# Kernel tuning notes

Hardware: AMD Instinct MI355X
Metric: run time of the kernel (lower is better)

## Reference

```python
import jax, jax.numpy as jnp
import numpy as np

CAUSAL = True


def setup_inputs() -> dict:
    key = jax.random.key(0)
    k1, k2, k3 = jax.random.split(key, 3)
    B, H, T, D = 2, 16, 2048, 64
    q = jax.random.normal(k1, (B, H, T, D), dtype=jnp.float32)
    k = jax.random.normal(k2, (B, H, T, D), dtype=jnp.float32)
    v = jax.random.normal(k3, (B, H, T, D), dtype=jnp.float32)
    return {"q": q, "k": k, "v": v}


def reference(q, k, v):
    # q,k,v: [B,H,T,D]
    d = q.shape[-1]
    scale = d ** -0.5
    dots = jnp.einsum('bhid,bhjd->bhij', q, k) * scale  # [B,H,T,T]
    if CAUSAL:
        t = q.shape[2]
        mask = jnp.triu(jnp.ones((t, t), dtype=bool), k=1)  # True above diagonal
        dots = jnp.where(mask, -jnp.inf, dots)
    attn = jax.nn.softmax(dots, axis=-1)
    # torch.einsum('bhjd,bhij->bhid', v, attn) == attn @ v
    return jnp.einsum('bhij,bhjd->bhid', attn, v)
```

## Files before the change

### kernel.cpp

```cpp
#include <hip/hip_runtime.h>
#include <hip/hip_bf16.h>

typedef unsigned short u16;
typedef unsigned int u32;
typedef __bf16 bf16x8 __attribute__((ext_vector_type(8)));
typedef short s16x4 __attribute__((ext_vector_type(4)));
typedef short s16x8 __attribute__((ext_vector_type(8)));
typedef float floatx4 __attribute__((ext_vector_type(4)));

#define T_SEQ 2048
#define HDIM 64
#define NBH 32

static __device__ __forceinline__ u16 f2b_rne(float x) {
    union { float f; u32 u; } c; c.f = x;
    u32 u = c.u;
    return (u16)((u + 0x7fffu + ((u >> 16) & 1u)) >> 16);
}
static __device__ __forceinline__ u16 f2b_trunc(float x) {
    union { float f; u32 u; } c; c.f = x;
    return (u16)(c.u >> 16);
}

#define GLOAD_LDS16(gp, lp)                                                      \
    __builtin_amdgcn_global_load_lds(                                            \
        (const __attribute__((address_space(1))) u32*)(gp),                      \
        (__attribute__((address_space(3))) u32*)(lp), 16, 0, 0)

__global__ __launch_bounds__(256) void prep(const float* __restrict__ k,
                                            const float* __restrict__ v,
                                            u16* __restrict__ kb,
                                            u16* __restrict__ vt) {
    __shared__ u16 tile[64][68];
    const int bh = blockIdx.y, t0 = blockIdx.x * 64;
    const int tid = threadIdx.x;

    const float* ksrc = k + ((size_t)bh * T_SEQ + t0) * HDIM;
    u16* kdst = kb + ((size_t)bh * T_SEQ + t0) * HDIM;
#pragma unroll
    for (int p = 0; p < 4; p++) {
        int idx = p * 256 + tid;
        float4 f = ((const float4*)ksrc)[idx];
        ushort4 o;
        o.x = f2b_rne(f.x); o.y = f2b_rne(f.y); o.z = f2b_rne(f.z); o.w = f2b_rne(f.w);
        ((ushort4*)kdst)[idx] = o;
    }

    const float* vsrc = v + ((size_t)bh * T_SEQ + t0) * HDIM;
#pragma unroll
    for (int p = 0; p < 4; p++) {
        int idx = p * 256 + tid;
        int r = idx >> 4, c4 = (idx & 15) * 4;
        float4 f = *(const float4*)(vsrc + r * HDIM + c4);
        tile[c4 + 0][r] = f2b_rne(f.x);
        tile[c4 + 1][r] = f2b_rne(f.y);
        tile[c4 + 2][r] = f2b_rne(f.z);
        tile[c4 + 3][r] = f2b_rne(f.w);
    }
    __syncthreads();
    u16* dst = vt + (size_t)bh * HDIM * T_SEQ + t0;
#pragma unroll
    for (int p = 0; p < 4; p++) {
        int idx = p * 256 + tid;
        int d = idx >> 4, c4 = (idx & 15) * 4;
        int t = c4 >> 4, qg = (c4 >> 2) & 3;
        int pos = qg * 16 + (t >> 1) * 8 + (t & 1) * 4;
        *(ushort4*)(dst + (size_t)d * T_SEQ + pos) = *(ushort4*)(&tile[d][c4]);
    }
}

__global__ __launch_bounds__(256, 2) void fattn(const float* __restrict__ q,
                                                const u16* __restrict__ kb,
                                                const u16* __restrict__ vtb,
                                                float* __restrict__ out) {
    __shared__ __align__(16) u16 Kl[2][64 * 64];
    __shared__ __align__(16) u16 Vl[2][64 * 64];

    const int bh = blockIdx.x;
    const int sr = blockIdx.y;
    const int st = (sr < 8) ? (2 * sr) : (2 * (15 - sr) + 1);
    const int tid = threadIdx.x;
    const int wave = tid >> 6, lane = tid & 63;
    const int l15 = lane & 15, quad = lane >> 4;

    const float* qp = q + (size_t)bh * T_SEQ * HDIM;
    const u16* kp = kb + (size_t)bh * T_SEQ * HDIM;
    const u16* vp = vtb + (size_t)bh * HDIM * T_SEQ;

    const int iters = 2 * st + 2;
    const int w32 = wave * 32;

    const int srow = wave * 8 + (lane >> 3);
    const int slot = lane & 7;
    const u16* kg0 = kp + srow * HDIM + (slot ^ (srow & 7)) * 8;
    const int vs = (slot - srow) & 7;
    const u16* vg0 = vp + (size_t)srow * T_SEQ + vs * 8;
    const u16* vg1 = vp + (size_t)(srow + 32) * T_SEQ + vs * 8;

    auto stage = [&](int j, int buf) {
        const u16* ks = kg0 + j * 64 * HDIM;
        u16* Kd = &Kl[buf][wave * 512];
        GLOAD_LDS16(ks, Kd);
        GLOAD_LDS16(ks + 32 * HDIM, Kd + 2048);
        u16* Vd = &Vl[buf][wave * 512];
        GLOAD_LDS16(vg0 + j * 64, Vd);
        GLOAD_LDS16(vg1 + j * 64, Vd + 2048);
    };

    stage(0, 0);

    const float SL2E = 0.125f * 1.44269504088896f;
    bf16x8 qf[2][2];
#pragma unroll
    for (int qn = 0; qn < 2; qn++) {
        const float* qrow = qp + (size_t)(st * 128 + w32 + qn * 16 + l15) * HDIM;
#pragma unroll
        for (int kc = 0; kc < 2; kc++) {
            const float4* p4 = (const float4*)(qrow + kc * 32 + quad * 8);
            float4 fa = p4[0], fb = p4[1];
            union { bf16x8 v; u16 s[8]; } cv;
            cv.s[0] = f2b_rne(fa.x * SL2E); cv.s[1] = f2b_rne(fa.y * SL2E);
            cv.s[2] = f2b_rne(fa.z * SL2E); cv.s[3] = f2b_rne(fa.w * SL2E);
            cv.s[4] = f2b_rne(fb.x * SL2E); cv.s[5] = f2b_rne(fb.y * SL2E);
            cv.s[6] = f2b_rne(fb.z * SL2E); cv.s[7] = f2b_rne(fb.w * SL2E);
            qf[qn][kc] = cv.v;
        }
    }

    floatx4 o_acc[2][4];
#pragma unroll
    for (int qn = 0; qn < 2; qn++)
#pragma unroll
        for (int dt = 0; dt < 4; dt++) o_acc[qn][dt] = (floatx4){0.f, 0.f, 0.f, 0.f};
    float lsum[2] = {0.f, 0.f};

    for (int j = 0; j < iters; ++j) {
        const int cur = j & 1;
        __syncthreads();

        if (j + 1 < iters) stage(j + 1, cur ^ 1);

        const int rel = j * 64 - st * 128;
        if (rel <= w32 + 31) {
            floatx4 sacc[2][4];
#pragma unroll
            for (int qn = 0; qn < 2; qn++)
#pragma unroll
                for (int kt = 0; kt < 4; kt++) sacc[qn][kt] = (floatx4){0.f, 0.f, 0.f, 0.f};
            const u16* Kc = Kl[cur];
#pragma unroll
            for (int kc = 0; kc < 2; kc++) {
#pragma unroll
                for (int kt = 0; kt < 4; kt++) {
                    int rk = kt * 16 + l15;
                    bf16x8 kf = *(const bf16x8*)(Kc + rk * 64 + ((kc * 4 + quad) ^ (rk & 7)) * 8);
                    sacc[0][kt] = __builtin_amdgcn_mfma_f32_16x16x32_bf16(kf, qf[0][kc], sacc[0][kt], 0, 0, 0);
                    sacc[1][kt] = __builtin_amdgcn_mfma_f32_16x16x32_bf16(kf, qf[1][kc], sacc[1][kt], 0, 0, 0);
                }
            }

            s16x4 pfrag[2][4];
            if (rel + 63 >= w32) {
#pragma unroll
                for (int qn = 0; qn < 2; qn++) {
                    const int gq = w32 + qn * 16 + l15;
#pragma unroll
                    for (int kt = 0; kt < 4; kt++) {
                        union { s16x4 v; u16 h[4]; } pk;
#pragma unroll
                        for (int rg = 0; rg < 4; rg++) {
                            float e = __builtin_amdgcn_exp2f(sacc[qn][kt][rg]);
                            if (rel + kt * 16 + quad * 4 + rg > gq) e = 0.f;
                            lsum[qn] += e;
                            pk.h[rg] = f2b_trunc(e);
                        }
                        pfrag[qn][kt] = pk.v;
                    }
                }
            } else {
#pragma unroll
                for (int qn = 0; qn < 2; qn++)
#pragma unroll
                    for (int kt = 0; kt < 4; kt++) {
                        union { s16x4 v; u16 h[4]; } pk;
#pragma unroll
                        for (int rg = 0; rg < 4; rg++) {
                            float e = __builtin_amdgcn_exp2f(sacc[qn][kt][rg]);
                            lsum[qn] += e;
                            pk.h[rg] = f2b_trunc(e);
                        }
                        pfrag[qn][kt] = pk.v;
                    }
            }

            const u16* Vc = Vl[cur];
#pragma unroll
            for (int tp = 0; tp < 2; tp++) {
#pragma unroll
                for (int dt = 0; dt < 4; dt++) {
                    int d = dt * 16 + l15;
                    int sl = (quad * 2 + tp + d) & 7;
                    s16x8 vf = *(const s16x8*)(Vc + d * 64 + sl * 8);
                    s16x4 vf0 = __builtin_shufflevector(vf, vf, 0, 1, 2, 3);
                    s16x4 vf1 = __builtin_shufflevector(vf, vf, 4, 5, 6, 7);
                    o_acc[0][dt] = __builtin_amdgcn_mfma_f32_16x16x16bf16_1k(pfrag[0][2 * tp], vf0, o_acc[0][dt], 0, 0, 0);
                    o_acc[0][dt] = __builtin_amdgcn_mfma_f32_16x16x16bf16_1k(pfrag[0][2 * tp + 1], vf1, o_acc[0][dt], 0, 0, 0);
                    o_acc[1][dt] = __builtin_amdgcn_mfma_f32_16x16x16bf16_1k(pfrag[1][2 * tp], vf0, o_acc[1][dt], 0, 0, 0);
                    o_acc[1][dt] = __builtin_amdgcn_mfma_f32_16x16x16bf16_1k(pfrag[1][2 * tp + 1], vf1, o_acc[1][dt], 0, 0, 0);
                }
            }
        }
    }

    float* op = out + (size_t)bh * T_SEQ * HDIM;
#pragma unroll
    for (int qn = 0; qn < 2; qn++) {
        float tot = lsum[qn];
        tot += __shfl_xor(tot, 16, 64);
        tot += __shfl_xor(tot, 32, 64);
#pragma unroll
        for (int rg = 0; rg < 4; rg++) {
            float inv = 1.0f / __shfl(tot, quad * 4 + rg, 64);
            size_t row = (size_t)(st * 128 + w32 + qn * 16 + quad * 4 + rg) * HDIM;
#pragma unroll
            for (int dt = 0; dt < 4; dt++)
                op[row + dt * 16 + l15] = o_acc[qn][dt][rg] * inv;
        }
    }
}

extern "C" void kernel_launch(void* const* d_in, const int* in_sizes, int n_in,
                              void* d_out, int out_size, void* d_ws, size_t ws_size,
                              hipStream_t stream) {
    const float* q = (const float*)d_in[0];
    const float* k = (const float*)d_in[1];
    const float* v = (const float*)d_in[2];
    float* out = (float*)d_out;

    u16* kb = (u16*)d_ws;
    u16* vt = kb + (size_t)NBH * T_SEQ * HDIM;

    prep<<<dim3(T_SEQ / 64, NBH), 256, 0, stream>>>(k, v, kb, vt);
    fattn<<<dim3(NBH, 16), 256, 0, stream>>>(q, kb, vt, out);
}
```

Before: 131.6 us.

## Split KV windows across waves with per-wave pipelines and LDS reduction

Each block now handles a 64-row query tile. Its four waves split the key/value sequence into interleaved 32-key windows instead of splitting the query rows. Each wave runs its own double-buffered global-to-LDS pipeline synchronised with waitcnt, so no block barriers are needed in the main loop, and the partial outputs and row sums are reduced through LDS at the end. The grid doubles to 32 query tiles per head, scheduled largest-first, and the V transpose layout changes to 32-key windows. This aims to remove per-iteration __syncthreads stalls and improve load balance. It costs a larger LDS footprint and an extra cross-wave reduction.

Result: faster. 124.2 us (-5.6%).

```diff
diff --git a/kernel.cpp b/kernel.cpp
--- a/kernel.cpp
+++ b/kernel.cpp
@@ -63,8 +63,8 @@
     for (int p = 0; p < 4; p++) {
         int idx = p * 256 + tid;
         int d = idx >> 4, c4 = (idx & 15) * 4;
-        int t = c4 >> 4, qg = (c4 >> 2) & 3;
-        int pos = qg * 16 + (t >> 1) * 8 + (t & 1) * 4;
+        int win = c4 >> 5, kt = (c4 >> 4) & 1, qg = (c4 >> 2) & 3;
+        int pos = win * 32 + qg * 8 + kt * 4;
         *(ushort4*)(dst + (size_t)d * T_SEQ + pos) = *(ushort4*)(&tile[d][c4]);
     }
 }
@@ -73,12 +73,10 @@
                                                 const u16* __restrict__ kb,
                                                 const u16* __restrict__ vtb,
                                                 float* __restrict__ out) {
-    __shared__ __align__(16) u16 Kl[2][64 * 64];
-    __shared__ __align__(16) u16 Vl[2][64 * 64];
+    __shared__ __align__(16) u16 smem[35328];
 
     const int bh = blockIdx.x;
-    const int sr = blockIdx.y;
-    const int st = (sr < 8) ? (2 * sr) : (2 * (15 - sr) + 1);
+    const int qt = 31 - (int)blockIdx.y;
     const int tid = threadIdx.x;
     const int wave = tid >> 6, lane = tid & 63;
     const int l15 = lane & 15, quad = lane >> 4;
@@ -87,33 +85,36 @@
     const u16* kp = kb + (size_t)bh * T_SEQ * HDIM;
     const u16* vp = vtb + (size_t)bh * HDIM * T_SEQ;
 
-    const int iters = 2 * st + 2;
-    const int w32 = wave * 32;
-
-    const int srow = wave * 8 + (lane >> 3);
-    const int slot = lane & 7;
-    const u16* kg0 = kp + srow * HDIM + (slot ^ (srow & 7)) * 8;
-    const int vs = (slot - srow) & 7;
-    const u16* vg0 = vp + (size_t)srow * T_SEQ + vs * 8;
-    const u16* vg1 = vp + (size_t)(srow + 32) * T_SEQ + vs * 8;
-
-    auto stage = [&](int j, int buf) {
-        const u16* ks = kg0 + j * 64 * HDIM;
-        u16* Kd = &Kl[buf][wave * 512];
-        GLOAD_LDS16(ks, Kd);
-        GLOAD_LDS16(ks + 32 * HDIM, Kd + 2048);
-        u16* Vd = &Vl[buf][wave * 512];
-        GLOAD_LDS16(vg0 + j * 64, Vd);
-        GLOAD_LDS16(vg1 + j * 64, Vd + 2048);
+    const int nwin = 2 * qt + 2;
+    const int nmy = (nwin > wave) ? ((nwin - wave + 3) >> 2) : 0;
+
+    u16* Tb = smem + wave * 8192;
+
+    const int ln3 = lane >> 3, ln7 = lane & 7;
+    const int ln2 = lane >> 2, ln3m = lane & 3;
+
+    auto stage = [&](int win, int b) {
+        const u16* ks = kp + win * 32 * HDIM;
+        u16* Kd = Tb + b * 2048;
+#pragma unroll
+        for (int l = 0; l < 4; l++) {
+            int kr = l * 8 + ln3;
+            GLOAD_LDS16(ks + kr * HDIM + (ln7 ^ (kr & 7)) * 8, Kd + l * 512);
+        }
+        const u16* vs = vp + win * 32;
+        u16* Vd = Tb + 4096 + b * 2048;
+#pragma unroll
+        for (int l = 0; l < 4; l++) {
+            int dr = l * 16 + ln2;
+            GLOAD_LDS16(vs + (size_t)dr * T_SEQ + ((ln3m - dr) & 3) * 8, Vd + l * 512);
+        }
     };
 
-    stage(0, 0);
-
     const float SL2E = 0.125f * 1.44269504088896f;
-    bf16x8 qf[2][2];
-#pragma unroll
-    for (int qn = 0; qn < 2; qn++) {
-        const float* qrow = qp + (size_t)(st * 128 + w32 + qn * 16 + l15) * HDIM;
+    bf16x8 qf[4][2];
+#pragma unroll
+    for (int qn = 0; qn < 4; qn++) {
+        const float* qrow = qp + (size_t)(qt * 64 + qn * 16 + l15) * HDIM;
 #pragma unroll
         for (int kc = 0; kc < 2; kc++) {
             const float4* p4 = (const float4*)(qrow + kc * 32 + quad * 8);
@@ -126,105 +127,140 @@
             qf[qn][kc] = cv.v;
         }
     }
-
-    floatx4 o_acc[2][4];
-#pragma unroll
-    for (int qn = 0; qn < 2; qn++)
+    asm volatile("s_waitcnt vmcnt(0)" ::: "memory");
+
+    if (nmy > 0) stage(wave, 0);
+    if (nmy > 1) stage(wave + 4, 1);
+
+    floatx4 o_acc[4][4];
+#pragma unroll
+    for (int qn = 0; qn < 4; qn++)
 #pragma unroll
         for (int dt = 0; dt < 4; dt++) o_acc[qn][dt] = (floatx4){0.f, 0.f, 0.f, 0.f};
-    float lsum[2] = {0.f, 0.f};
-
-    for (int j = 0; j < iters; ++j) {
-        const int cur = j & 1;
-        __syncthreads();
-
-        if (j + 1 < iters) stage(j + 1, cur ^ 1);
-
-        const int rel = j * 64 - st * 128;
-        if (rel <= w32 + 31) {
-            floatx4 sacc[2][4];
-#pragma unroll
-            for (int qn = 0; qn < 2; qn++)
-#pragma unroll
-                for (int kt = 0; kt < 4; kt++) sacc[qn][kt] = (floatx4){0.f, 0.f, 0.f, 0.f};
-            const u16* Kc = Kl[cur];
-#pragma unroll
-            for (int kc = 0; kc < 2; kc++) {
-#pragma unroll
-                for (int kt = 0; kt < 4; kt++) {
-                    int rk = kt * 16 + l15;
-                    bf16x8 kf = *(const bf16x8*)(Kc + rk * 64 + ((kc * 4 + quad) ^ (rk & 7)) * 8);
-                    sacc[0][kt] = __builtin_amdgcn_mfma_f32_16x16x32_bf16(kf, qf[0][kc], sacc[0][kt], 0, 0, 0);
-                    sacc[1][kt] = __builtin_amdgcn_mfma_f32_16x16x32_bf16(kf, qf[1][kc], sacc[1][kt], 0, 0, 0);
+    float lsum[4] = {0.f, 0.f, 0.f, 0.f};
+
+    for (int i = 0; i < nmy; i++) {
+        const int win = wave + 4 * i;
+        const int b = i & 1;
+        if (i + 1 < nmy) { asm volatile("s_waitcnt vmcnt(8)" ::: "memory"); }
+        else             { asm volatile("s_waitcnt vmcnt(0)" ::: "memory"); }
+
+        const u16* Kc = Tb + b * 2048;
+        bf16x8 kf[2][2];
+#pragma unroll
+        for (int kt = 0; kt < 2; kt++) {
+            int kr = kt * 16 + l15;
+#pragma unroll
+            for (int kc = 0; kc < 2; kc++)
+                kf[kt][kc] = *(const bf16x8*)(Kc + kr * 64 + (((kc * 4 + quad) ^ (kr & 7)) * 8));
+        }
+        const u16* Vc = Tb + 4096 + b * 2048;
+        s16x8 vfull[4];
+#pragma unroll
+        for (int dt = 0; dt < 4; dt++) {
+            int d = dt * 16 + l15;
+            vfull[dt] = *(const s16x8*)(Vc + d * 32 + ((quad + d) & 3) * 8);
+        }
+        asm volatile("s_waitcnt lgkmcnt(0)" ::: "memory");
+        if (i + 2 < nmy) stage(wave + 4 * (i + 2), b);
+
+        floatx4 sacc[2][4];
+#pragma unroll
+        for (int kt = 0; kt < 2; kt++)
+#pragma unroll
+            for (int qn = 0; qn < 4; qn++) sacc[kt][qn] = (floatx4){0.f, 0.f, 0.f, 0.f};
+#pragma unroll
+        for (int kc = 0; kc < 2; kc++)
+#pragma unroll
+            for (int kt = 0; kt < 2; kt++)
+#pragma unroll
+                for (int qn = 0; qn < 4; qn++)
+                    sacc[kt][qn] = __builtin_amdgcn_mfma_f32_16x16x32_bf16(
+                        kf[kt][kc], qf[qn][kc], sacc[kt][qn], 0, 0, 0);
+
+        s16x4 pf[2][4];
+        if (win >= 2 * qt) {
+            const int base = (win - 2 * qt) * 32;
+#pragma unroll
+            for (int kt = 0; kt < 2; kt++)
+#pragma unroll
+                for (int qn = 0; qn < 4; qn++) {
+                    union { s16x4 v; u16 h[4]; } pk;
+#pragma unroll
+                    for (int rg = 0; rg < 4; rg++) {
+                        float e = __builtin_amdgcn_exp2f(sacc[kt][qn][rg]);
+                        if (base + kt * 16 + quad * 4 + rg > qn * 16 + l15) e = 0.f;
+                        lsum[qn] += e;
+                        pk.h[rg] = f2b_trunc(e);
+                    }
+                    pf[kt][qn] = pk.v;
                 }
+        } else {
+#pragma unroll
+            for (int kt = 0; kt < 2; kt++)
+#pragma unroll
+                for (int qn = 0; qn < 4; qn++) {
+                    union { s16x4 v; u16 h[4]; } pk;
+#pragma unroll
+                    for (int rg = 0; rg < 4; rg++) {
+                        float e = __builtin_amdgcn_exp2f(sacc[kt][qn][rg]);
+                        lsum[qn] += e;
+                        pk.h[rg] = f2b_trunc(e);
+                    }
+                    pf[kt][qn] = pk.v;
+                }
+        }
+
+#pragma unroll
+        for (int dt = 0; dt < 4; dt++) {
+            s16x4 v0 = __builtin_shufflevector(vfull[dt], vfull[dt], 0, 1, 2, 3);
+            s16x4 v1 = __builtin_shufflevector(vfull[dt], vfull[dt], 4, 5, 6, 7);
+#pragma unroll
+            for (int qn = 0; qn < 4; qn++) {
+                o_acc[qn][dt] = __builtin_amdgcn_mfma_f32_16x16x16bf16_1k(pf[0][qn], v0, o_acc[qn][dt], 0, 0, 0);
+                o_acc[qn][dt] = __builtin_amdgcn_mfma_f32_16x16x16bf16_1k(pf[1][qn], v1, o_acc[qn][dt], 0, 0, 0);
             }
-
-            s16x4 pfrag[2][4];
-            if (rel + 63 >= w32) {
-#pragma unroll
-                for (int qn = 0; qn < 2; qn++) {
-                    const int gq = w32 + qn * 16 + l15;
-#pragma unroll
-                    for (int kt = 0; kt < 4; kt++) {
-                        union { s16x4 v; u16 h[4]; } pk;
-#pragma unroll
-                        for (int rg = 0; rg < 4; rg++) {
-                            float e = __builtin_amdgcn_exp2f(sacc[qn][kt][rg]);
-                            if (rel + kt * 16 + quad * 4 + rg > gq) e = 0.f;
-                            lsum[qn] += e;
-                            pk.h[rg] = f2b_trunc(e);
-                        }
-                        pfrag[qn][kt] = pk.v;
-                    }
-                }
-            } else {
-#pragma unroll
-                for (int qn = 0; qn < 2; qn++)
-#pragma unroll
-                    for (int kt = 0; kt < 4; kt++) {
-                        union { s16x4 v; u16 h[4]; } pk;
-#pragma unroll
-                        for (int rg = 0; rg < 4; rg++) {
-                            float e = __builtin_amdgcn_exp2f(sacc[qn][kt][rg]);
-                            lsum[qn] += e;
-                            pk.h[rg] = f2b_trunc(e);
-                        }
-                        pfrag[qn][kt] = pk.v;
-                    }
-            }
-
-            const u16* Vc = Vl[cur];
-#pragma unroll
-            for (int tp = 0; tp < 2; tp++) {
-#pragma unroll
-                for (int dt = 0; dt < 4; dt++) {
-                    int d = dt * 16 + l15;
-                    int sl = (quad * 2 + tp + d) & 7;
-                    s16x8 vf = *(const s16x8*)(Vc + d * 64 + sl * 8);
-                    s16x4 vf0 = __builtin_shufflevector(vf, vf, 0, 1, 2, 3);
-                    s16x4 vf1 = __builtin_shufflevector(vf, vf, 4, 5, 6, 7);
-                    o_acc[0][dt] = __builtin_amdgcn_mfma_f32_16x16x16bf16_1k(pfrag[0][2 * tp], vf0, o_acc[0][dt], 0, 0, 0);
-                    o_acc[0][dt] = __builtin_amdgcn_mfma_f32_16x16x16bf16_1k(pfrag[0][2 * tp + 1], vf1, o_acc[0][dt], 0, 0, 0);
-                    o_acc[1][dt] = __builtin_amdgcn_mfma_f32_16x16x16bf16_1k(pfrag[1][2 * tp], vf0, o_acc[1][dt], 0, 0, 0);
-                    o_acc[1][dt] = __builtin_amdgcn_mfma_f32_16x16x16bf16_1k(pfrag[1][2 * tp + 1], vf1, o_acc[1][dt], 0, 0, 0);
-                }
-            }
-        }
-    }
-
-    float* op = out + (size_t)bh * T_SEQ * HDIM;
-#pragma unroll
-    for (int qn = 0; qn < 2; qn++) {
-        float tot = lsum[qn];
-        tot += __shfl_xor(tot, 16, 64);
-        tot += __shfl_xor(tot, 32, 64);
-#pragma unroll
-        for (int rg = 0; rg < 4; rg++) {
-            float inv = 1.0f / __shfl(tot, quad * 4 + rg, 64);
-            size_t row = (size_t)(st * 128 + w32 + qn * 16 + quad * 4 + rg) * HDIM;
-#pragma unroll
-            for (int dt = 0; dt < 4; dt++)
-                op[row + dt * 16 + l15] = o_acc[qn][dt][rg] * inv;
+        }
+    }
+
+    __syncthreads();
+    float* oq = (float*)smem + wave * 4352;
+#pragma unroll
+    for (int qn = 0; qn < 4; qn++)
+#pragma unroll
+        for (int dt = 0; dt < 4; dt++)
+#pragma unroll
+            for (int rg = 0; rg < 4; rg++)
+                oq[(qn * 16 + quad * 4 + rg) * 68 + dt * 16 + l15] = o_acc[qn][dt][rg];
+
+    float* lsa = (float*)smem + 17408;
+#pragma unroll
+    for (int qn = 0; qn < 4; qn++) {
+        float t = lsum[qn];
+        t += __shfl_xor(t, 16, 64);
+        t += __shfl_xor(t, 32, 64);
+        if (quad == 0) lsa[wave * 64 + qn * 16 + l15] = t;
+    }
+    __syncthreads();
+
+    {
+        const int qr = wave * 16 + l15;
+        float lt = lsa[qr] + lsa[64 + qr] + lsa[128 + qr] + lsa[192 + qr];
+        float inv = 1.0f / lt;
+        const float* q0 = (float*)smem + qr * 68 + quad * 16;
+        float* op = out + ((size_t)bh * T_SEQ + qt * 64 + qr) * HDIM + quad * 16;
+#pragma unroll
+        for (int c = 0; c < 4; c++) {
+            float4 s0 = *(const float4*)(q0 + c * 4);
+            float4 s1 = *(const float4*)(q0 + 4352 + c * 4);
+            float4 s2 = *(const float4*)(q0 + 8704 + c * 4);
+            float4 s3 = *(const float4*)(q0 + 13056 + c * 4);
+            float4 r;
+            r.x = (s0.x + s1.x + s2.x + s3.x) * inv;
+            r.y = (s0.y + s1.y + s2.y + s3.y) * inv;
+            r.z = (s0.z + s1.z + s2.z + s3.z) * inv;
+            r.w = (s0.w + s1.w + s2.w + s3.w) * inv;
+            *(float4*)(op + c * 4) = r;
         }
     }
 }
@@ -241,5 +277,5 @@
     u16* vt = kb + (size_t)NBH * T_SEQ * HDIM;
 
     prep<<<dim3(T_SEQ / 64, NBH), 256, 0, stream>>>(k, v, kb, vt);
-    fattn<<<dim3(NBH, 16), 256, 0, stream>>>(q, kb, vt, out);
-}
+    fattn<<<dim3(NBH, 32), 256, 0, stream>>>(q, kb, vt, out);
+}
```

## Pair a long and a short causal query tile per block for balanced work

Applied to the files above, without the earlier changes.

Each block now processes two 64-row query tiles, the long tile 31-p and the short tile p, instead of one 128-row tile. Each wave owns 16 rows of each tile. K/V tiles are shared, and both tiles are computed only while the short tile is still active, so every block does about the same causal work. Causal masking is applied only on the diagonal tile, and the bf16 packing of probabilities uses a byte-permute instruction. The cost is more total K/V tile loads across the grid, and there are separate code paths for dual-tile and single-tile iterations.

Result: no change. 131.8 us (+0.2%).

```diff
diff --git a/kernel.cpp b/kernel.cpp
--- a/kernel.cpp
+++ b/kernel.cpp
@@ -17,9 +17,9 @@
     u32 u = c.u;
     return (u16)((u + 0x7fffu + ((u >> 16) & 1u)) >> 16);
 }
-static __device__ __forceinline__ u16 f2b_trunc(float x) {
+static __device__ __forceinline__ u32 fbits(float x) {
     union { float f; u32 u; } c; c.f = x;
-    return (u16)(c.u >> 16);
+    return c.u;
 }
 
 #define GLOAD_LDS16(gp, lp)                                                      \
@@ -77,8 +77,10 @@
     __shared__ __align__(16) u16 Vl[2][64 * 64];
 
     const int bh = blockIdx.x;
-    const int sr = blockIdx.y;
-    const int st = (sr < 8) ? (2 * sr) : (2 * (15 - sr) + 1);
+    const int p = blockIdx.y;
+    const int qtb = 31 - p;
+    const int qts = p;
+    const int iters = qtb + 1;
     const int tid = threadIdx.x;
     const int wave = tid >> 6, lane = tid & 63;
     const int l15 = lane & 15, quad = lane >> 4;
@@ -86,9 +88,6 @@
     const float* qp = q + (size_t)bh * T_SEQ * HDIM;
     const u16* kp = kb + (size_t)bh * T_SEQ * HDIM;
     const u16* vp = vtb + (size_t)bh * HDIM * T_SEQ;
-
-    const int iters = 2 * st + 2;
-    const int w32 = wave * 32;
 
     const int srow = wave * 8 + (lane >> 3);
     const int slot = lane & 7;
@@ -113,7 +112,8 @@
     bf16x8 qf[2][2];
 #pragma unroll
     for (int qn = 0; qn < 2; qn++) {
-        const float* qrow = qp + (size_t)(st * 128 + w32 + qn * 16 + l15) * HDIM;
+        const int base = (qn ? qts : qtb) * 64 + wave * 16;
+        const float* qrow = qp + (size_t)(base + l15) * HDIM;
 #pragma unroll
         for (int kc = 0; kc < 2; kc++) {
             const float4* p4 = (const float4*)(qrow + kc * 32 + quad * 8);
@@ -133,6 +133,7 @@
 #pragma unroll
         for (int dt = 0; dt < 4; dt++) o_acc[qn][dt] = (floatx4){0.f, 0.f, 0.f, 0.f};
     float lsum[2] = {0.f, 0.f};
+    const floatx4 ZERO4 = {0.f, 0.f, 0.f, 0.f};
 
     for (int j = 0; j < iters; ++j) {
         const int cur = j & 1;
@@ -140,75 +141,89 @@
 
         if (j + 1 < iters) stage(j + 1, cur ^ 1);
 
-        const int rel = j * 64 - st * 128;
-        if (rel <= w32 + 31) {
-            floatx4 sacc[2][4];
-#pragma unroll
-            for (int qn = 0; qn < 2; qn++)
-#pragma unroll
-                for (int kt = 0; kt < 4; kt++) sacc[qn][kt] = (floatx4){0.f, 0.f, 0.f, 0.f};
-            const u16* Kc = Kl[cur];
-#pragma unroll
-            for (int kc = 0; kc < 2; kc++) {
-#pragma unroll
-                for (int kt = 0; kt < 4; kt++) {
-                    int rk = kt * 16 + l15;
-                    bf16x8 kf = *(const bf16x8*)(Kc + rk * 64 + ((kc * 4 + quad) ^ (rk & 7)) * 8);
-                    sacc[0][kt] = __builtin_amdgcn_mfma_f32_16x16x32_bf16(kf, qf[0][kc], sacc[0][kt], 0, 0, 0);
-                    sacc[1][kt] = __builtin_amdgcn_mfma_f32_16x16x32_bf16(kf, qf[1][kc], sacc[1][kt], 0, 0, 0);
+        const u16* Kc = Kl[cur];
+        const u16* Vc = Vl[cur];
+        const bool dual = (j <= qts);
+
+        floatx4 sacc[2][4];
+        if (dual) {
+#pragma unroll
+            for (int kt = 0; kt < 4; kt++) {
+                int rk = kt * 16 + l15;
+                bf16x8 kf0 = *(const bf16x8*)(Kc + rk * 64 + ((quad) ^ (rk & 7)) * 8);
+                sacc[0][kt] = __builtin_amdgcn_mfma_f32_16x16x32_bf16(kf0, qf[0][0], ZERO4, 0, 0, 0);
+                sacc[1][kt] = __builtin_amdgcn_mfma_f32_16x16x32_bf16(kf0, qf[1][0], ZERO4, 0, 0, 0);
+                bf16x8 kf1 = *(const bf16x8*)(Kc + rk * 64 + ((4 + quad) ^ (rk & 7)) * 8);
+                sacc[0][kt] = __builtin_amdgcn_mfma_f32_16x16x32_bf16(kf1, qf[0][1], sacc[0][kt], 0, 0, 0);
+                sacc[1][kt] = __builtin_amdgcn_mfma_f32_16x16x32_bf16(kf1, qf[1][1], sacc[1][kt], 0, 0, 0);
+            }
+        } else {
+#pragma unroll
+            for (int kt = 0; kt < 4; kt++) {
+                int rk = kt * 16 + l15;
+                bf16x8 kf0 = *(const bf16x8*)(Kc + rk * 64 + ((quad) ^ (rk & 7)) * 8);
+                sacc[0][kt] = __builtin_amdgcn_mfma_f32_16x16x32_bf16(kf0, qf[0][0], ZERO4, 0, 0, 0);
+                bf16x8 kf1 = *(const bf16x8*)(Kc + rk * 64 + ((4 + quad) ^ (rk & 7)) * 8);
+                sacc[0][kt] = __builtin_amdgcn_mfma_f32_16x16x32_bf16(kf1, qf[0][1], sacc[0][kt], 0, 0, 0);
+            }
+        }
+
+        s16x4 pf[2][4];
+        const int nq = dual ? 2 : 1;
+#pragma unroll
+        for (int qn = 0; qn < 2; qn++) {
+            if (qn >= nq) break;
+            const bool diag = (j == (qn ? qts : qtb));
+            const int rhs = wave * 16 + l15;
+#pragma unroll
+            for (int kt = 0; kt < 4; kt++) {
+                float e0 = __builtin_amdgcn_exp2f(sacc[qn][kt][0]);
+                float e1 = __builtin_amdgcn_exp2f(sacc[qn][kt][1]);
+                float e2 = __builtin_amdgcn_exp2f(sacc[qn][kt][2]);
+                float e3 = __builtin_amdgcn_exp2f(sacc[qn][kt][3]);
+                if (diag) {
+                    int kl = kt * 16 + quad * 4;
+                    if (kl + 0 > rhs) e0 = 0.f;
+                    if (kl + 1 > rhs) e1 = 0.f;
+                    if (kl + 2 > rhs) e2 = 0.f;
+                    if (kl + 3 > rhs) e3 = 0.f;
                 }
+                lsum[qn] += (e0 + e1) + (e2 + e3);
+                union { s16x4 v; u32 w[2]; } pk;
+                pk.w[0] = __builtin_amdgcn_perm(fbits(e1), fbits(e0), 0x07060302u);
+                pk.w[1] = __builtin_amdgcn_perm(fbits(e3), fbits(e2), 0x07060302u);
+                pf[qn][kt] = pk.v;
             }
-
-            s16x4 pfrag[2][4];
-            if (rel + 63 >= w32) {
-#pragma unroll
-                for (int qn = 0; qn < 2; qn++) {
-                    const int gq = w32 + qn * 16 + l15;
-#pragma unroll
-                    for (int kt = 0; kt < 4; kt++) {
-                        union { s16x4 v; u16 h[4]; } pk;
-#pragma unroll
-                        for (int rg = 0; rg < 4; rg++) {
-                            float e = __builtin_amdgcn_exp2f(sacc[qn][kt][rg]);
-                            if (rel + kt * 16 + quad * 4 + rg > gq) e = 0.f;
-                            lsum[qn] += e;
-                            pk.h[rg] = f2b_trunc(e);
-                        }
-                        pfrag[qn][kt] = pk.v;
-                    }
-                }
-            } else {
-#pragma unroll
-                for (int qn = 0; qn < 2; qn++)
-#pragma unroll
-                    for (int kt = 0; kt < 4; kt++) {
-                        union { s16x4 v; u16 h[4]; } pk;
-#pragma unroll
-                        for (int rg = 0; rg < 4; rg++) {
-                            float e = __builtin_amdgcn_exp2f(sacc[qn][kt][rg]);
-                            lsum[qn] += e;
-                            pk.h[rg] = f2b_trunc(e);
-                        }
-                        pfrag[qn][kt] = pk.v;
-                    }
-            }
-
-            const u16* Vc = Vl[cur];
-#pragma unroll
-            for (int tp = 0; tp < 2; tp++) {
+        }
+
+        if (dual) {
+#pragma unroll
+            for (int tp = 0; tp < 2; tp++)
 #pragma unroll
                 for (int dt = 0; dt < 4; dt++) {
                     int d = dt * 16 + l15;
                     int sl = (quad * 2 + tp + d) & 7;
-                    s16x8 vf = *(const s16x8*)(Vc + d * 64 + sl * 8);
-                    s16x4 vf0 = __builtin_shufflevector(vf, vf, 0, 1, 2, 3);
-                    s16x4 vf1 = __builtin_shufflevector(vf, vf, 4, 5, 6, 7);
-                    o_acc[0][dt] = __builtin_amdgcn_mfma_f32_16x16x16bf16_1k(pfrag[0][2 * tp], vf0, o_acc[0][dt], 0, 0, 0);
-                    o_acc[0][dt] = __builtin_amdgcn_mfma_f32_16x16x16bf16_1k(pfrag[0][2 * tp + 1], vf1, o_acc[0][dt], 0, 0, 0);
-                    o_acc[1][dt] = __builtin_amdgcn_mfma_f32_16x16x16bf16_1k(pfrag[1][2 * tp], vf0, o_acc[1][dt], 0, 0, 0);
-                    o_acc[1][dt] = __builtin_amdgcn_mfma_f32_16x16x16bf16_1k(pfrag[1][2 * tp + 1], vf1, o_acc[1][dt], 0, 0, 0);
+                    s16x8 vfx = *(const s16x8*)(Vc + d * 64 + sl * 8);
+                    s16x4 v0 = __builtin_shufflevector(vfx, vfx, 0, 1, 2, 3);
+                    s16x4 v1 = __builtin_shufflevector(vfx, vfx, 4, 5, 6, 7);
+                    o_acc[0][dt] = __builtin_amdgcn_mfma_f32_16x16x16bf16_1k(pf[0][2 * tp], v0, o_acc[0][dt], 0, 0, 0);
+                    o_acc[0][dt] = __builtin_amdgcn_mfma_f32_16x16x16bf16_1k(pf[0][2 * tp + 1], v1, o_acc[0][dt], 0, 0, 0);
+                    o_acc[1][dt] = __builtin_amdgcn_mfma_f32_16x16x16bf16_1k(pf[1][2 * tp], v0, o_acc[1][dt], 0, 0, 0);
+                    o_acc[1][dt] = __builtin_amdgcn_mfma_f32_16x16x16bf16_1k(pf[1][2 * tp + 1], v1, o_acc[1][dt], 0, 0, 0);
                 }
-            }
+        } else {
+#pragma unroll
+            for (int tp = 0; tp < 2; tp++)
+#pragma unroll
+                for (int dt = 0; dt < 4; dt++) {
+                    int d = dt * 16 + l15;
+                    int sl = (quad * 2 + tp + d) & 7;
+                    s16x8 vfx = *(const s16x8*)(Vc + d * 64 + sl * 8);
+                    s16x4 v0 = __builtin_shufflevector(vfx, vfx, 0, 1, 2, 3);
+                    s16x4 v1 = __builtin_shufflevector(vfx, vfx, 4, 5, 6, 7);
+                    o_acc[0][dt] = __builtin_amdgcn_mfma_f32_16x16x16bf16_1k(pf[0][2 * tp], v0, o_acc[0][dt], 0, 0, 0);
+                    o_acc[0][dt] = __builtin_amdgcn_mfma_f32_16x16x16bf16_1k(pf[0][2 * tp + 1], v1, o_acc[0][dt], 0, 0, 0);
+                }
         }
     }
 
@@ -218,10 +233,11 @@
         float tot = lsum[qn];
         tot += __shfl_xor(tot, 16, 64);
         tot += __shfl_xor(tot, 32, 64);
+        const int base = (qn ? qts : qtb) * 64 + wave * 16;
 #pragma unroll
         for (int rg = 0; rg < 4; rg++) {
             float inv = 1.0f / __shfl(tot, quad * 4 + rg, 64);
-            size_t row = (size_t)(st * 128 + w32 + qn * 16 + quad * 4 + rg) * HDIM;
+            size_t row = (size_t)(base + quad * 4 + rg) * HDIM;
 #pragma unroll
             for (int dt = 0; dt < 4; dt++)
                 op[row + dt * 16 + l15] = o_acc[qn][dt][rg] * inv;
```
